# Kernel optimization log

Measured on AMD Instinct MI355X. Metric: run time of the kernel, lower is better.

Reference implementation:

```python
import jax, jax.numpy as jnp
import numpy as np
import math

ALPHA = 0.1
LAMDA = 0.5
N_NODES = 100000
N_EDGES = 1600000
NLAYER = 4


def gcn_norm(edge_index, num_nodes):
    # symmetric GCN normalization with added self loops (fill value 1.0)
    loop = jnp.arange(num_nodes, dtype=edge_index.dtype)
    row = jnp.concatenate([edge_index[0], loop])
    col = jnp.concatenate([edge_index[1], loop])
    w = jnp.ones(row.shape[0], dtype=jnp.float32)
    deg = jax.ops.segment_sum(w, col, num_segments=num_nodes)
    dis = jnp.where(deg > 0, jax.lax.rsqrt(deg), 0.0)
    return row, col, dis[row] * w * dis[col]


def gcnii_conv(x, h0, w1, w2, beta, row, col, norm_w, num_nodes):
    # support/initial residual mixing (GCNII)
    support = (1.0 - beta) * (1.0 - ALPHA) * x + beta * (x @ w1)
    initial = (1.0 - beta) * ALPHA * h0 + beta * (h0 @ w2)
    # gather-scale-scatter: out[i] = sum_e norm_w[e] * support[row[e]] at col[e]
    msgs = norm_w[:, None] * support[row]
    agg = jax.ops.segment_sum(msgs, col, num_segments=num_nodes)
    return agg + initial


def setup_inputs() -> dict:
    key = jax.random.key(0)
    ks = jax.random.split(key, 8)
    # edges without self loops: col = (row + offset) % N, offset in [1, N-1]
    row = jax.random.randint(ks[0], (N_EDGES,), 0, N_NODES)
    off = jax.random.randint(ks[1], (N_EDGES,), 1, N_NODES)
    col = (row + off) % N_NODES
    edge_index = jnp.stack([row, col]).astype(jnp.int64)
    g = 0.1
    return {
        "x": jax.random.normal(ks[2], (N_NODES, 17), jnp.float32),
        "edge_index": edge_index,
        "W_in": jax.random.normal(ks[3], (17, 64), jnp.float32) * g,
        "b_in": jnp.zeros((64,), jnp.float32),
        "W1": jax.random.normal(ks[4], (NLAYER, 64, 64), jnp.float32) * g,
        "W2": jax.random.normal(ks[5], (NLAYER, 64, 64), jnp.float32) * g,
        "W_out": jax.random.normal(ks[6], (64, 2), jnp.float32) * g,
        "b_out": jnp.zeros((2,), jnp.float32),
    }


def reference(x, edge_index, W_in, b_in, W1, W2, W_out, b_out):
    num_nodes = x.shape[0]
    row, col, norm_w = gcn_norm(edge_index, num_nodes)
    # eval mode: dropout is identity
    h = jax.nn.relu(x @ W_in + b_in)
    h0 = h
    for i in range(NLAYER):
        beta = math.log(LAMDA / (i + 1) + 1.0)
        h = jax.nn.relu(gcnii_conv(h, h0, W1[i], W2[i], beta, row, col, norm_w, num_nodes))
    logits = h @ W_out + b_out
    return jax.nn.log_softmax(logits, axis=1)
```

## Files before the change

### kernel.cpp

```cpp
#include <hip/hip_runtime.h>
#include <math.h>

#define ALPHA_C 0.1f
#define EPB 4096

typedef __attribute__((ext_vector_type(4))) float f32x4;
typedef __attribute__((ext_vector_type(8))) short bf16x8;

__device__ __forceinline__ float readlane_f(float v, int l) {
    return __int_as_float(__builtin_amdgcn_readlane(__float_as_int(v), l));
}

__device__ __forceinline__ unsigned short bf16_rtne(float f) {
    unsigned u = __float_as_uint(f);
    unsigned r = (u + 0x7FFFu + ((u >> 16) & 1u)) >> 16;
    return (unsigned short)r;
}

__device__ __forceinline__ float bflo(unsigned v) { return __uint_as_float(v << 16); }
__device__ __forceinline__ float bfhi(unsigned v) { return __uint_as_float(v & 0xFFFF0000u); }

__global__ void k_rhist(const int* __restrict__ col, int E, int span,
                        int* __restrict__ rangecount) {
    __shared__ int l[64];
    int tid = threadIdx.x;
    if (tid < 64) l[tid] = 0;
    __syncthreads();
    int base = blockIdx.x * EPB;
#pragma unroll
    for (int it = 0; it < 16; ++it) {
        int e = base + it * 256 + tid;
        if (e < E) atomicAdd(&l[(unsigned)col[e] / (unsigned)span], 1);
    }
    __syncthreads();
    if (tid < 64 && l[tid]) atomicAdd(&rangecount[tid], l[tid]);
}

__global__ void k_rscan(const int* __restrict__ rangecount,
                        int* __restrict__ rangeoffs, int E) {
    __shared__ int s[64];
    int tid = threadIdx.x;
    int v = rangecount[tid];
    s[tid] = v;
    __syncthreads();
    for (int d = 1; d < 64; d <<= 1) {
        int t = (tid >= d) ? s[tid - d] : 0;
        __syncthreads();
        s[tid] += t;
        __syncthreads();
    }
    rangeoffs[tid] = s[tid] - v;
    if (tid == 63) rangeoffs[64] = E;
}

__global__ void k_binA(const int* __restrict__ row, const int* __restrict__ col,
                       const int* __restrict__ rangeoffs, int* __restrict__ gcur,
                       unsigned* __restrict__ staged, int E, int span) {
    __shared__ int lrun[64];
    int tid = threadIdx.x;
    int base = blockIdx.x * EPB;
    if (tid < 64) lrun[tid] = 0;
    __syncthreads();
#pragma unroll
    for (int it = 0; it < 16; ++it) {
        int e = base + it * 256 + tid;
        if (e < E) atomicAdd(&lrun[(unsigned)col[e] / (unsigned)span], 1);
    }
    __syncthreads();
    if (tid < 64) {
        int cnt = lrun[tid];
        int gb = cnt ? atomicAdd(&gcur[tid], cnt) : 0;
        lrun[tid] = rangeoffs[tid] + gb;
    }
    __syncthreads();
#pragma unroll
    for (int it = 0; it < 16; ++it) {
        int e = base + it * 256 + tid;
        if (e < E) {
            int c = col[e];
            int r = (unsigned)c / (unsigned)span;
            int pos = atomicAdd(&lrun[r], 1);
            staged[pos] = ((unsigned)row[e] << 11) | (unsigned)(c - r * span);
        }
    }
}

__global__ void k_binB(const unsigned* __restrict__ staged, const int* __restrict__ rangeoffs,
                       int* __restrict__ offs, float* __restrict__ dinv,
                       int* __restrict__ srcarr, int N, int span) {
    __shared__ int lcnt[1600];
    __shared__ int partial[256];
    int r = blockIdx.x;
    int tid = threadIdx.x;
    int nstart = r * span;
    if (nstart >= N) return;
    int nend = nstart + span; if (nend > N) nend = N;
    int cnt = nend - nstart;
    int estart = rangeoffs[r], eend = rangeoffs[r + 1];
    for (int t = tid; t < cnt; t += 256) lcnt[t] = 0;
    __syncthreads();
    for (int e = estart + tid; e < eend; e += 256)
        atomicAdd(&lcnt[staged[e] & 0x7FFu], 1);
    __syncthreads();
    int chunk = (cnt + 255) / 256;
    int c0 = tid * chunk; if (c0 > cnt) c0 = cnt;
    int c1 = c0 + chunk;  if (c1 > cnt) c1 = cnt;
    int sum = 0;
    for (int t = c0; t < c1; ++t) sum += lcnt[t];
    partial[tid] = sum;
    __syncthreads();
    for (int d = 1; d < 256; d <<= 1) {
        int t = (tid >= d) ? partial[tid - d] : 0;
        __syncthreads();
        partial[tid] += t;
        __syncthreads();
    }
    int run = estart + partial[tid] - sum;
    for (int t = c0; t < c1; ++t) {
        int c = lcnt[t];
        lcnt[t] = run;
        offs[nstart + t] = run;
        dinv[nstart + t] = rsqrtf(1.0f + (float)c);
        run += c;
    }
    if (nend == N && tid == 0) offs[N] = eend;
    __syncthreads();
    for (int e = estart + tid; e < eend; e += 256) {
        unsigned m = staged[e];
        int idx = atomicAdd(&lcnt[m & 0x7FFu], 1);
        srcarr[idx] = (int)(m >> 11);
    }
}

__global__ void k_wfold(const float* __restrict__ W1, const float* __restrict__ W2,
                        float beta, float c2, unsigned short* __restrict__ wf) {
    int idx = blockIdx.x * 256 + threadIdx.x;
    if (idx < 8192) {
        int n = idx >> 7, k = idx & 127;
        float w = (k < 64) ? beta * W1[k * 64 + n]
                           : beta * W2[(k - 64) * 64 + n] + (((k - 64) == n) ? c2 : 0.0f);
        wf[idx] = bf16_rtne(w);
    }
}

__global__ void k_in(const float* __restrict__ x, const float* __restrict__ Win,
                     const float* __restrict__ bin, const float* __restrict__ dinv,
                     unsigned short* __restrict__ h0b, unsigned short* __restrict__ g,
                     int N) {
    int lane = threadIdx.x & 63;
    int wave = (blockIdx.x * blockDim.x + threadIdx.x) >> 6;
    int nwaves = (gridDim.x * blockDim.x) >> 6;
    float wreg[17];
#pragma unroll
    for (int k = 0; k < 17; ++k) wreg[k] = Win[k * 64 + lane];
    float breg = bin[lane];
    for (int i = wave; i < N; i += nwaves) {
        float xv = (lane < 17) ? x[i * 17 + lane] : 0.0f;
        float acc = breg;
#pragma unroll
        for (int k = 0; k < 17; ++k) acc += readlane_f(xv, k) * wreg[k];
        float r = fmaxf(acc, 0.0f);
        h0b[(size_t)i * 64 + lane] = bf16_rtne(r);
        g[(size_t)i * 64 + lane] = bf16_rtne(dinv[i] * r);
    }
}

template <int MODE>
__global__ void k_gmix(const uint2* __restrict__ gp2,
                       const unsigned short* __restrict__ h0b,
                       const unsigned short* __restrict__ wf,
                       const float* __restrict__ dinv, const int* __restrict__ offs,
                       const int* __restrict__ srcarr, float c1,
                       const float* __restrict__ Wout, const float* __restrict__ bout,
                       float* __restrict__ out, unsigned short* __restrict__ og16,
                       int N, int ntiles) {
    __shared__ float atile_s[4][16][68];
    int lane = threadIdx.x & 63;
    int wv = threadIdx.x >> 6;
    float (*atile)[68] = atile_s[wv];
    int r = lane & 15, q = lane >> 4;
    int t = (blockIdx.x * blockDim.x + threadIdx.x) >> 6;
    if (t >= ntiles) return;

    int rl = lane & 15;
    int koff = (lane >> 4) * 8;
    bf16x8 bfrag[4][4];
#pragma unroll
    for (int c = 0; c < 4; ++c)
#pragma unroll
        for (int ks = 0; ks < 4; ++ks)
            bfrag[c][ks] = *(const bf16x8*)&wf[(c * 16 + rl) * 128 + ks * 32 + koff];

    for (int ii = 0; ii < 16; ++ii) {
        int i = t * 16 + ii; if (i >= N) i = N - 1;
        int e0 = offs[i], e1 = offs[i + 1];
        float a0 = 0.0f, a1 = 0.0f, a2 = 0.0f, a3 = 0.0f;
        for (int base = e0; base < e1; base += 32) {
            int idx[8];
            uint2 v[8];
#pragma unroll
            for (int u = 0; u < 8; ++u) {
                int eo = base + u * 4 + q;
                idx[u] = srcarr[eo < e1 ? eo : e1 - 1];
            }
#pragma unroll
            for (int u = 0; u < 8; ++u) v[u] = gp2[(size_t)idx[u] * 16 + r];
#pragma unroll
            for (int u = 0; u < 8; ++u) {
                bool ok = (base + u * 4 + q) < e1;
                a0 += ok ? bflo(v[u].x) : 0.0f;
                a1 += ok ? bfhi(v[u].x) : 0.0f;
                a2 += ok ? bflo(v[u].y) : 0.0f;
                a3 += ok ? bfhi(v[u].y) : 0.0f;
            }
        }
        a0 += __shfl_xor(a0, 16, 64); a0 += __shfl_xor(a0, 32, 64);
        a1 += __shfl_xor(a1, 16, 64); a1 += __shfl_xor(a1, 32, 64);
        a2 += __shfl_xor(a2, 16, 64); a2 += __shfl_xor(a2, 32, 64);
        a3 += __shfl_xor(a3, 16, 64); a3 += __shfl_xor(a3, 32, 64);
        if (q == 0) {
            uint2 sv = gp2[(size_t)i * 16 + r];
            float di = dinv[i];
            f32x4 w = {di * (a0 + bflo(sv.x)), di * (a1 + bfhi(sv.x)),
                       di * (a2 + bflo(sv.y)), di * (a3 + bfhi(sv.y))};
            *(f32x4*)&atile[ii][4 * r] = w;
            if (r == 0) atile[ii][66] = di;
        }
    }

    int grow = t * 16 + rl; if (grow >= N) grow = N - 1;
    f32x4 acc[4];
#pragma unroll
    for (int c = 0; c < 4; ++c) acc[c] = (f32x4){0.f, 0.f, 0.f, 0.f};
#pragma unroll
    for (int ks = 0; ks < 4; ++ks) {
        bf16x8 af;
        if (ks < 2) {
            const float* sp = &atile[rl][ks * 32 + koff];
            f32x4 lo = *(const f32x4*)sp;
            f32x4 hi = *(const f32x4*)(sp + 4);
#pragma unroll
            for (int j = 0; j < 4; ++j) af[j] = (short)bf16_rtne(lo[j]);
#pragma unroll
            for (int j = 0; j < 4; ++j) af[4 + j] = (short)bf16_rtne(hi[j]);
        } else {
            af = *(const bf16x8*)&h0b[(size_t)grow * 64 + (ks - 2) * 32 + koff];
        }
#pragma unroll
        for (int c = 0; c < 4; ++c)
            acc[c] = __builtin_amdgcn_mfma_f32_16x16x32_bf16(af, bfrag[c][ks], acc[c], 0, 0, 0);
    }

    if (MODE == 0) {
#pragma unroll
        for (int c = 0; c < 4; ++c) {
            int col = c * 16 + rl;
#pragma unroll
            for (int qq = 0; qq < 4; ++qq) {
                int row16 = (lane >> 4) * 4 + qq;
                int gr = t * 16 + row16;
                if (gr < N) {
                    float v = c1 * atile[row16][col] + acc[c][qq];
                    float rr = fmaxf(v, 0.0f);
                    og16[(size_t)gr * 64 + col] = bf16_rtne(atile[row16][66] * rr);
                }
            }
        }
    } else {
        float w0c[4], w1c[4];
#pragma unroll
        for (int c = 0; c < 4; ++c) {
            int col = c * 16 + rl;
            w0c[c] = Wout[col * 2 + 0];
            w1c[c] = Wout[col * 2 + 1];
        }
        float b0 = bout[0], b1 = bout[1];
        float hq[4][4];
#pragma unroll
        for (int c = 0; c < 4; ++c) {
            int col = c * 16 + rl;
#pragma unroll
            for (int qq = 0; qq < 4; ++qq) {
                int row16 = (lane >> 4) * 4 + qq;
                hq[c][qq] = fmaxf(c1 * atile[row16][col] + acc[c][qq], 0.0f);
            }
        }
#pragma unroll
        for (int qq = 0; qq < 4; ++qq) {
            float p0 = hq[0][qq] * w0c[0] + hq[1][qq] * w0c[1]
                     + hq[2][qq] * w0c[2] + hq[3][qq] * w0c[3];
            float p1 = hq[0][qq] * w1c[0] + hq[1][qq] * w1c[1]
                     + hq[2][qq] * w1c[2] + hq[3][qq] * w1c[3];
#pragma unroll
            for (int d = 1; d < 16; d <<= 1) {
                p0 += __shfl_xor(p0, d, 64);
                p1 += __shfl_xor(p1, d, 64);
            }
            int row16 = (lane >> 4) * 4 + qq;
            int gr = t * 16 + row16;
            if (rl == 0 && gr < N) {
                float l0 = p0 + b0, l1 = p1 + b1;
                float m = fmaxf(l0, l1);
                float lse = m + logf(expf(l0 - m) + expf(l1 - m));
                out[(size_t)gr * 2 + 0] = l0 - lse;
                out[(size_t)gr * 2 + 1] = l1 - lse;
            }
        }
    }
}

extern "C" void kernel_launch(void* const* d_in, const int* in_sizes, int n_in,
                              void* d_out, int out_size, void* d_ws, size_t ws_size,
                              hipStream_t stream) {
    const float* x    = (const float*)d_in[0];
    const int*   ei   = (const int*)d_in[1];
    const float* Win  = (const float*)d_in[2];
    const float* bin  = (const float*)d_in[3];
    const float* W1   = (const float*)d_in[4];
    const float* W2   = (const float*)d_in[5];
    const float* Wout = (const float*)d_in[6];
    const float* bout = (const float*)d_in[7];
    float* out = (float*)d_out;

    const int N = in_sizes[0] / 17;
    const int E = in_sizes[1] / 2;
    const int* rowp = ei;
    const int* colp = ei + E;
    const int span = (N + 63) / 64;

    char* p = (char*)d_ws;
    auto alloc = [&](size_t bytes) -> char* {
        char* r = p;
        p += (bytes + 255) & ~(size_t)255;
        return r;
    };
    int*      offs   = (int*)alloc((size_t)(N + 1) * sizeof(int));
    float*    dinv   = (float*)alloc((size_t)N * sizeof(float));
    int*      rc_gc  = (int*)alloc(128 * sizeof(int));
    int*      roffs  = (int*)alloc(65 * sizeof(int));
    int*      srcarr = (int*)alloc((size_t)E * sizeof(int));
    unsigned short* wfold = (unsigned short*)alloc(4 * 8192 * sizeof(unsigned short));
    size_t gbytes  = (size_t)N * 64 * sizeof(unsigned short);
    size_t stbytes = (size_t)E * sizeof(unsigned);
    char*  stg    = alloc(stbytes > gbytes ? stbytes : gbytes);
    unsigned short* h0b = (unsigned short*)alloc(gbytes);
    unsigned short* gA  = (unsigned short*)alloc(gbytes);
    unsigned*       staged = (unsigned*)stg;
    unsigned short* gB     = (unsigned short*)stg;

    int* rangecount = rc_gc;
    int* gcur       = rc_gc + 64;
    hipMemsetAsync(rc_gc, 0, 128 * sizeof(int), stream);

    const int TB = 256;
    const int nbA = (E + EPB - 1) / EPB;

    k_rhist<<<nbA, TB, 0, stream>>>(colp, E, span, rangecount);
    k_rscan<<<1, 64, 0, stream>>>(rangecount, roffs, E);
    k_binA<<<nbA, TB, 0, stream>>>(rowp, colp, roffs, gcur, staged, E, span);
    k_binB<<<64, TB, 0, stream>>>(staged, roffs, offs, dinv, srcarr, N, span);

    k_in<<<2048, TB, 0, stream>>>(x, Win, bin, dinv, h0b, gA, N);
    for (int l = 0; l < 4; ++l) {
        float beta = logf(0.5f / (float)(l + 1) + 1.0f);
        float c2 = (1.0f - beta) * ALPHA_C;
        k_wfold<<<32, TB, 0, stream>>>(W1 + (size_t)l * 4096, W2 + (size_t)l * 4096,
                                       beta, c2, wfold + (size_t)l * 8192);
    }

    const int ntiles = (N + 15) >> 4;
    const int nbG = (ntiles + 3) / 4;

    for (int l = 0; l < 4; ++l) {
        float beta = logf(0.5f / (float)(l + 1) + 1.0f);
        float c1 = (1.0f - beta) * (1.0f - ALPHA_C);
        const unsigned short* gin  = (l & 1) ? gB : gA;
        unsigned short*       gout = (l & 1) ? gA : gB;
        if (l < 3)
            k_gmix<0><<<nbG, TB, 0, stream>>>((const uint2*)gin, h0b,
                                              wfold + (size_t)l * 8192,
                                              dinv, offs, srcarr, c1,
                                              nullptr, nullptr, nullptr, gout,
                                              N, ntiles);
        else
            k_gmix<1><<<nbG, TB, 0, stream>>>((const uint2*)gin, h0b,
                                              wfold + (size_t)l * 8192,
                                              dinv, offs, srcarr, c1,
                                              Wout, bout, out, nullptr,
                                              N, ntiles);
    }
}
```

Baseline: 445.5 us.

## Bin edges into fixed-capacity buckets, dropping histogram pass; widen ranges to 256

```diff
diff --git a/kernel.cpp b/kernel.cpp
--- a/kernel.cpp
+++ b/kernel.cpp
@@ -3,6 +3,8 @@
 
 #define ALPHA_C 0.1f
 #define EPB 4096
+#define NR 256
+#define RCAP 8192
 
 typedef __attribute__((ext_vector_type(4))) float f32x4;
 typedef __attribute__((ext_vector_type(8))) short bf16x8;
@@ -20,46 +22,13 @@
 __device__ __forceinline__ float bflo(unsigned v) { return __uint_as_float(v << 16); }
 __device__ __forceinline__ float bfhi(unsigned v) { return __uint_as_float(v & 0xFFFF0000u); }
 
-__global__ void k_rhist(const int* __restrict__ col, int E, int span,
-                        int* __restrict__ rangecount) {
-    __shared__ int l[64];
-    int tid = threadIdx.x;
-    if (tid < 64) l[tid] = 0;
-    __syncthreads();
-    int base = blockIdx.x * EPB;
-#pragma unroll
-    for (int it = 0; it < 16; ++it) {
-        int e = base + it * 256 + tid;
-        if (e < E) atomicAdd(&l[(unsigned)col[e] / (unsigned)span], 1);
-    }
-    __syncthreads();
-    if (tid < 64 && l[tid]) atomicAdd(&rangecount[tid], l[tid]);
-}
-
-__global__ void k_rscan(const int* __restrict__ rangecount,
-                        int* __restrict__ rangeoffs, int E) {
-    __shared__ int s[64];
-    int tid = threadIdx.x;
-    int v = rangecount[tid];
-    s[tid] = v;
-    __syncthreads();
-    for (int d = 1; d < 64; d <<= 1) {
-        int t = (tid >= d) ? s[tid - d] : 0;
-        __syncthreads();
-        s[tid] += t;
-        __syncthreads();
-    }
-    rangeoffs[tid] = s[tid] - v;
-    if (tid == 63) rangeoffs[64] = E;
-}
-
 __global__ void k_binA(const int* __restrict__ row, const int* __restrict__ col,
-                       const int* __restrict__ rangeoffs, int* __restrict__ gcur,
-                       unsigned* __restrict__ staged, int E, int span) {
-    __shared__ int lrun[64];
+                       int* __restrict__ gcur, unsigned* __restrict__ staged,
+                       int E, int span) {
+    __shared__ int lrun[NR];
     int tid = threadIdx.x;
     int base = blockIdx.x * EPB;
-    if (tid < 64) lrun[tid] = 0;
+    lrun[tid] = 0;
     __syncthreads();
 #pragma unroll
     for (int it = 0; it < 16; ++it) {
@@ -67,10 +36,10 @@
         if (e < E) atomicAdd(&lrun[(unsigned)col[e] / (unsigned)span], 1);
     }
     __syncthreads();
-    if (tid < 64) {
+    {
         int cnt = lrun[tid];
         int gb = cnt ? atomicAdd(&gcur[tid], cnt) : 0;
-        lrun[tid] = rangeoffs[tid] + gb;
+        lrun[tid] = tid * RCAP + gb;
     }
     __syncthreads();
 #pragma unroll
@@ -80,27 +49,46 @@
             int c = col[e];
             int r = (unsigned)c / (unsigned)span;
             int pos = atomicAdd(&lrun[r], 1);
-            staged[pos] = ((unsigned)row[e] << 11) | (unsigned)(c - r * span);
-        }
-    }
-}
-
-__global__ void k_binB(const unsigned* __restrict__ staged, const int* __restrict__ rangeoffs,
+            staged[pos] = ((unsigned)row[e] << 9) | (unsigned)(c - r * span);
+        }
+    }
+}
+
+__global__ void k_escan(const int* __restrict__ gcur, int* __restrict__ rangeoffs, int E) {
+    __shared__ int s[NR];
+    int tid = threadIdx.x;
+    int v = gcur[tid];
+    s[tid] = v;
+    __syncthreads();
+    for (int d = 1; d < NR; d <<= 1) {
+        int t = (tid >= d) ? s[tid - d] : 0;
+        __syncthreads();
+        s[tid] += t;
+        __syncthreads();
+    }
+    rangeoffs[tid] = s[tid] - v;
+    if (tid == NR - 1) rangeoffs[NR] = E;
+}
+
+__global__ void k_binB(const unsigned* __restrict__ staged, const int* __restrict__ gcur,
+                       const int* __restrict__ rangeoffs,
                        int* __restrict__ offs, float* __restrict__ dinv,
                        int* __restrict__ srcarr, int N, int span) {
-    __shared__ int lcnt[1600];
+    __shared__ int lcnt[512];
     __shared__ int partial[256];
     int r = blockIdx.x;
     int tid = threadIdx.x;
     int nstart = r * span;
-    if (nstart >= N) return;
+    if (nstart >= N) { if (tid == 0 && r == NR - 1) offs[N] = rangeoffs[NR]; return; }
     int nend = nstart + span; if (nend > N) nend = N;
     int cnt = nend - nstart;
-    int estart = rangeoffs[r], eend = rangeoffs[r + 1];
+    int estart = rangeoffs[r];
+    int ecnt = gcur[r];
+    const unsigned* st = staged + (size_t)r * RCAP;
     for (int t = tid; t < cnt; t += 256) lcnt[t] = 0;
     __syncthreads();
-    for (int e = estart + tid; e < eend; e += 256)
-        atomicAdd(&lcnt[staged[e] & 0x7FFu], 1);
+    for (int e = tid; e < ecnt; e += 256)
+        atomicAdd(&lcnt[st[e] & 0x1FFu], 1);
     __syncthreads();
     int chunk = (cnt + 255) / 256;
     int c0 = tid * chunk; if (c0 > cnt) c0 = cnt;
@@ -123,22 +111,27 @@
         dinv[nstart + t] = rsqrtf(1.0f + (float)c);
         run += c;
     }
-    if (nend == N && tid == 0) offs[N] = eend;
-    __syncthreads();
-    for (int e = estart + tid; e < eend; e += 256) {
-        unsigned m = staged[e];
-        int idx = atomicAdd(&lcnt[m & 0x7FFu], 1);
-        srcarr[idx] = (int)(m >> 11);
+    if (nend == N && tid == 0) offs[N] = rangeoffs[NR];
+    __syncthreads();
+    for (int e = tid; e < ecnt; e += 256) {
+        unsigned m = st[e];
+        int idx = atomicAdd(&lcnt[m & 0x1FFu], 1);
+        srcarr[idx] = (int)(m >> 9);
     }
 }
 
 __global__ void k_wfold(const float* __restrict__ W1, const float* __restrict__ W2,
-                        float beta, float c2, unsigned short* __restrict__ wf) {
+                        unsigned short* __restrict__ wf) {
     int idx = blockIdx.x * 256 + threadIdx.x;
-    if (idx < 8192) {
-        int n = idx >> 7, k = idx & 127;
-        float w = (k < 64) ? beta * W1[k * 64 + n]
-                           : beta * W2[(k - 64) * 64 + n] + (((k - 64) == n) ? c2 : 0.0f);
+    if (idx < 4 * 8192) {
+        int l = idx >> 13;
+        int n = (idx >> 7) & 63, k = idx & 127;
+        float beta = logf(0.5f / (float)(l + 1) + 1.0f);
+        float c2 = (1.0f - beta) * ALPHA_C;
+        const float* Wl1 = W1 + (size_t)l * 4096;
+        const float* Wl2 = W2 + (size_t)l * 4096;
+        float w = (k < 64) ? beta * Wl1[k * 64 + n]
+                           : beta * Wl2[(k - 64) * 64 + n] + (((k - 64) == n) ? c2 : 0.0f);
         wf[idx] = bf16_rtne(w);
     }
 }
@@ -326,7 +319,7 @@
     const int E = in_sizes[1] / 2;
     const int* rowp = ei;
     const int* colp = ei + E;
-    const int span = (N + 63) / 64;
+    const int span = (N + NR - 1) / NR;
 
     char* p = (char*)d_ws;
     auto alloc = [&](size_t bytes) -> char* {
@@ -334,39 +327,29 @@
         p += (bytes + 255) & ~(size_t)255;
         return r;
     };
-    int*      offs   = (int*)alloc((size_t)(N + 1) * sizeof(int));
-    float*    dinv   = (float*)alloc((size_t)N * sizeof(float));
-    int*      rc_gc  = (int*)alloc(128 * sizeof(int));
-    int*      roffs  = (int*)alloc(65 * sizeof(int));
-    int*      srcarr = (int*)alloc((size_t)E * sizeof(int));
+    int*      offs      = (int*)alloc((size_t)(N + 1) * sizeof(int));
+    float*    dinv      = (float*)alloc((size_t)N * sizeof(float));
+    int*      gcur      = (int*)alloc(NR * sizeof(int));
+    int*      rangeoffs = (int*)alloc((NR + 1) * sizeof(int));
+    int*      srcarr    = (int*)alloc((size_t)E * sizeof(int));
     unsigned short* wfold = (unsigned short*)alloc(4 * 8192 * sizeof(unsigned short));
-    size_t gbytes  = (size_t)N * 64 * sizeof(unsigned short);
-    size_t stbytes = (size_t)E * sizeof(unsigned);
-    char*  stg    = alloc(stbytes > gbytes ? stbytes : gbytes);
+    unsigned* staged    = (unsigned*)alloc((size_t)NR * RCAP * sizeof(unsigned));
+    size_t gbytes = (size_t)N * 64 * sizeof(unsigned short);
     unsigned short* h0b = (unsigned short*)alloc(gbytes);
     unsigned short* gA  = (unsigned short*)alloc(gbytes);
-    unsigned*       staged = (unsigned*)stg;
-    unsigned short* gB     = (unsigned short*)stg;
-
-    int* rangecount = rc_gc;
-    int* gcur       = rc_gc + 64;
-    hipMemsetAsync(rc_gc, 0, 128 * sizeof(int), stream);
+    unsigned short* gB  = (unsigned short*)alloc(gbytes);
+
+    hipMemsetAsync(gcur, 0, NR * sizeof(int), stream);
 
     const int TB = 256;
     const int nbA = (E + EPB - 1) / EPB;
 
-    k_rhist<<<nbA, TB, 0, stream>>>(colp, E, span, rangecount);
-    k_rscan<<<1, 64, 0, stream>>>(rangecount, roffs, E);
-    k_binA<<<nbA, TB, 0, stream>>>(rowp, colp, roffs, gcur, staged, E, span);
-    k_binB<<<64, TB, 0, stream>>>(staged, roffs, offs, dinv, srcarr, N, span);
-
+    k_binA<<<nbA, TB, 0, stream>>>(rowp, colp, gcur, staged, E, span);
+    k_escan<<<1, NR, 0, stream>>>(gcur, rangeoffs, E);
+    k_binB<<<NR, TB, 0, stream>>>(staged, gcur, rangeoffs, offs, dinv, srcarr, N, span);
+
+    k_wfold<<<128, TB, 0, stream>>>(W1, W2, wfold);
     k_in<<<2048, TB, 0, stream>>>(x, Win, bin, dinv, h0b, gA, N);
-    for (int l = 0; l < 4; ++l) {
-        float beta = logf(0.5f / (float)(l + 1) + 1.0f);
-        float c2 = (1.0f - beta) * ALPHA_C;
-        k_wfold<<<32, TB, 0, stream>>>(W1 + (size_t)l * 4096, W2 + (size_t)l * 4096,
-                                       beta, c2, wfold + (size_t)l * 8192);
-    }
 
     const int ntiles = (N + 15) >> 4;
     const int nbG = (ntiles + 3) / 4;
```

Result: faster. 389.0 us (-12.7%).
